# Kernel tuning notes

Hardware: AMD Instinct MI355X
Metric: run time of the kernel (lower is better)

Reference implementation:

```python
import jax, jax.numpy as jnp
import numpy as np

VOXEL_SIZE = 0.2   # matches init voxel_size
N_STEPS = 192      # fixed-step ray marching (vectorized stand-in for per-ray DDA)


def setup_inputs() -> dict:
    key = jax.random.key(0)
    k1, k2, k3, k4 = jax.random.split(key, 4)
    B, T, Z, Y, X = 1, 6, 32, 512, 512
    N = 65536
    # non-negative occupancy density (sigma)
    sigma = jax.random.uniform(k1, (B, T, Z, Y, X), jnp.float32) * 2.0
    # sensor origin near grid center per future frame, coords in (x, y, z) voxel units
    center = jnp.array([X / 2.0, Y / 2.0, Z / 2.0], jnp.float32)
    org = center + jax.random.uniform(k2, (B, T, 3), jnp.float32) * 2.0
    # point cloud endpoints uniformly inside the grid
    pcd = jax.random.uniform(k3, (B, N, 3), jnp.float32) * jnp.array([X - 1.0, Y - 1.0, Z - 1.0], jnp.float32)
    tindex = jax.random.randint(k4, (B, N), 0, T).astype(jnp.int32)
    return {"dense_occ_sigma": sigma, "future_org": org, "future_pcd": pcd, "future_tindex": tindex}


def _render(sigma, org, pcd, tindex):
    # sigma: [B,T,Z,Y,X]; org: [B,T,3]; pcd: [B,N,3]; tindex: [B,N]
    B, T, Z, Y, X = sigma.shape
    b_idx = jnp.arange(B)[:, None]                      # [B,1]
    org_pts = org[b_idx, tindex]                        # [B,N,3] origin per ray
    ray = pcd - org_pts                                 # [B,N,3]
    gt = jnp.sqrt(jnp.sum(ray * ray, axis=-1))          # [B,N] gt distance (voxel units)
    dirn = ray / jnp.maximum(gt[..., None], 1e-8)
    # midpoint samples along each ray
    frac = (jnp.arange(N_STEPS, dtype=jnp.float32) + 0.5) / N_STEPS  # [S]
    t = gt[..., None] * frac                            # [B,N,S]
    pos = org_pts[..., None, :] + dirn[..., None, :] * t[..., None]  # [B,N,S,3]
    ix = jnp.floor(pos[..., 0]).astype(jnp.int32)
    iy = jnp.floor(pos[..., 1]).astype(jnp.int32)
    iz = jnp.floor(pos[..., 2]).astype(jnp.int32)
    inside = (ix >= 0) & (ix < X) & (iy >= 0) & (iy < Y) & (iz >= 0) & (iz < Z)
    ixc = jnp.clip(ix, 0, X - 1)
    iyc = jnp.clip(iy, 0, Y - 1)
    izc = jnp.clip(iz, 0, Z - 1)
    s = sigma[b_idx[..., None], tindex[..., None], izc, iyc, ixc]    # [B,N,S] voxel gathers
    s = jnp.where(inside, s, 0.0)
    delta = (gt / N_STEPS)[..., None]                   # [B,N,1] step length
    tau = s * delta                                     # optical thickness per step
    cum = jnp.cumsum(tau, axis=-1)                      # [B,N,S]
    trans = jnp.exp(-(cum - tau))                       # transmittance before each step
    alpha = 1.0 - jnp.exp(-tau)
    w = trans * alpha                                   # termination prob per step
    # expected termination distance; residual transmittance terminates at ray end
    pred = jnp.sum(w * t, axis=-1) + jnp.exp(-cum[..., -1]) * gt
    return pred, gt


def reference(dense_occ_sigma, future_org, future_pcd, future_tindex):
    pred, gt = _render(dense_occ_sigma, future_org, future_pcd, future_tindex)
    # NaN/Inf cleanup as in the wrapper (gt masked with pred's invalid mask)
    bad = jnp.isinf(pred) | jnp.isnan(pred)
    pred = jnp.where(bad, 0.0, pred)
    gt = jnp.where(bad, 0.0, gt)
    return pred * VOXEL_SIZE, gt * VOXEL_SIZE
```

## Files before the change

### kernel.cpp

```cpp
#include <hip/hip_runtime.h>
#include <math.h>

#define TFRAMES 6
#define ZD 32
#define YD 512
#define XD 512
#define NRAYS 65536
#define NSTEPS 192
#define VOXEL 0.2f

__global__ __launch_bounds__(256) void volrender_kernel(
    const float* __restrict__ sigma,
    const float* __restrict__ org,
    const float* __restrict__ pcd,
    const int*   __restrict__ tindex,
    float*       __restrict__ out)
{
    const int lane = threadIdx.x & 63;
    const int ray  = (blockIdx.x * blockDim.x + threadIdx.x) >> 6;
    if (ray >= NRAYS) return;

    const int   t  = tindex[ray];
    const float px = pcd[ray * 3 + 0];
    const float py = pcd[ray * 3 + 1];
    const float pz = pcd[ray * 3 + 2];
    const float ox = org[t * 3 + 0];
    const float oy = org[t * 3 + 1];
    const float oz = org[t * 3 + 2];

    const float rx = px - ox, ry = py - oy, rz = pz - oz;
    float gt = sqrtf(rx * rx + ry * ry + rz * rz);
    const float invgt = 1.0f / fmaxf(gt, 1e-8f);
    const float dx = rx * invgt, dy = ry * invgt, dz = rz * invgt;
    const float delta = gt * (1.0f / NSTEPS);

    const int base = t * (ZD * YD * XD);

    float tau[3], tt[3];
#pragma unroll
    for (int j = 0; j < 3; ++j) {
        const int   s    = lane * 3 + j;
        const float frac = ((float)s + 0.5f) * (1.0f / NSTEPS);
        const float tcur = gt * frac;
        tt[j] = tcur;
        const float x = ox + dx * tcur;
        const float y = oy + dy * tcur;
        const float z = oz + dz * tcur;
        const int ix = (int)floorf(x);
        const int iy = (int)floorf(y);
        const int iz = (int)floorf(z);
        const bool inside = (ix >= 0) & (ix < XD) & (iy >= 0) & (iy < YD) &
                            (iz >= 0) & (iz < ZD);
        const int ixc = min(max(ix, 0), XD - 1);
        const int iyc = min(max(iy, 0), YD - 1);
        const int izc = min(max(iz, 0), ZD - 1);
        const float sv = sigma[base + (izc * YD + iyc) * XD + ixc];
        tau[j] = inside ? sv * delta : 0.0f;
    }

    const float p0 = tau[0];
    const float p1 = p0 + tau[1];
    const float p2 = p1 + tau[2];

    float incl = p2;
#pragma unroll
    for (int off = 1; off < 64; off <<= 1) {
        const float u = __shfl_up(incl, off);
        if (lane >= off) incl += u;
    }
    const float excl  = incl - p2;
    const float total = __shfl(incl, 63);

    const float e0 = __expf(-excl);
    const float e1 = __expf(-(excl + p0));
    const float e2 = __expf(-(excl + p1));
    const float e3 = __expf(-(excl + p2));
    float pr = (e0 - e1) * tt[0] + (e1 - e2) * tt[1] + (e2 - e3) * tt[2];

#pragma unroll
    for (int off = 32; off >= 1; off >>= 1)
        pr += __shfl_xor(pr, off);

    float pred = pr + __expf(-total) * gt;

    if (isnan(pred) || isinf(pred)) { pred = 0.0f; gt = 0.0f; }

    if (lane == 0) {
        out[ray]         = pred * VOXEL;
        out[NRAYS + ray] = gt * VOXEL;
    }
}

extern "C" void kernel_launch(void* const* d_in, const int* in_sizes, int n_in,
                              void* d_out, int out_size, void* d_ws, size_t ws_size,
                              hipStream_t stream) {
    const float* sigma  = (const float*)d_in[0];
    const float* org    = (const float*)d_in[1];
    const float* pcd    = (const float*)d_in[2];
    const int*   tindex = (const int*)d_in[3];
    float*       out    = (float*)d_out;

    const int threads = 256;
    const int blocks  = (NRAYS * 64) / threads;
    volrender_kernel<<<blocks, threads, 0, stream>>>(sigma, org, pcd, tindex, out);
}
```

Measured before the change: 329.9 us.

## Bin rays by frame and endpoint tile and remap blocks for cache locality

Adds a counting-sort pass that bins rays by time frame and coarse 64x64 XY tile of the endpoint, producing a permutation that the render kernel uses to order ray processing. Block indices are also swizzled across 8 groups so that concurrently running blocks touch spatially similar rays. The goal is better L2/MALL reuse of sigma gathers, since rays in the same frame and region sample overlapping voxels near the shared origin and endpoint. This costs four extra small kernel launches, atomics and an indirection load per ray, and only takes effect when workspace is provided.

```diff
diff --git a/kernel.cpp b/kernel.cpp
--- a/kernel.cpp
+++ b/kernel.cpp
@@ -9,16 +9,57 @@
 #define NSTEPS 192
 #define VOXEL 0.2f
 
+#define NBINS (TFRAMES * 64)
+
+
+__global__ void zero_counts_kernel(int* counts) {
+    if (threadIdx.x < NBINS) counts[threadIdx.x] = 0;
+}
+
+__device__ __forceinline__ int ray_bin(const float* pcd, const int* tindex, int i) {
+    const int   t  = tindex[i];
+    const float px = pcd[i * 3 + 0];
+    const float py = pcd[i * 3 + 1];
+    const int ex = min(7, max(0, (int)(px * (1.0f / 64.0f))));
+    const int ey = min(7, max(0, (int)(py * (1.0f / 64.0f))));
+    return (t * 8 + ey) * 8 + ex;
+}
+
+__global__ __launch_bounds__(256) void hist_kernel(
+    const float* __restrict__ pcd, const int* __restrict__ tindex, int* counts) {
+    const int i = blockIdx.x * 256 + threadIdx.x;
+    atomicAdd(&counts[ray_bin(pcd, tindex, i)], 1);
+}
+
+__global__ void prefix_kernel(const int* __restrict__ counts, int* offsets) {
+    if (threadIdx.x == 0 && blockIdx.x == 0) {
+        int acc = 0;
+        for (int b = 0; b < NBINS; ++b) { offsets[b] = acc; acc += counts[b]; }
+    }
+}
+
+__global__ __launch_bounds__(256) void scatter_kernel(
+    const float* __restrict__ pcd, const int* __restrict__ tindex,
+    int* offsets, int* __restrict__ perm) {
+    const int i = blockIdx.x * 256 + threadIdx.x;
+    const int pos = atomicAdd(&offsets[ray_bin(pcd, tindex, i)], 1);
+    perm[pos] = i;
+}
+
+
 __global__ __launch_bounds__(256) void volrender_kernel(
     const float* __restrict__ sigma,
     const float* __restrict__ org,
     const float* __restrict__ pcd,
     const int*   __restrict__ tindex,
+    const int*   __restrict__ perm,
     float*       __restrict__ out)
 {
     const int lane = threadIdx.x & 63;
-    const int ray  = (blockIdx.x * blockDim.x + threadIdx.x) >> 6;
-    if (ray >= NRAYS) return;
+    const int lb   = (blockIdx.x & 7) * 2048 + (blockIdx.x >> 3);
+    const int slot = lb * 4 + (threadIdx.x >> 6);
+    if (slot >= NRAYS) return;
+    const int ray = perm ? perm[slot] : slot;
 
     const int   t  = tindex[ray];
     const float px = pcd[ray * 3 + 0];
@@ -100,7 +141,19 @@
     const int*   tindex = (const int*)d_in[3];
     float*       out    = (float*)d_out;
 
+    const size_t need = (size_t)(NBINS * 2 + NRAYS) * sizeof(int);
+    int* perm = nullptr;
+    if (d_ws && ws_size >= need) {
+        int* counts  = (int*)d_ws;
+        int* offsets = counts + NBINS;
+        perm         = offsets + NBINS;
+        zero_counts_kernel<<<1, NBINS, 0, stream>>>(counts);
+        hist_kernel<<<NRAYS / 256, 256, 0, stream>>>(pcd, tindex, counts);
+        prefix_kernel<<<1, 64, 0, stream>>>(counts, offsets);
+        scatter_kernel<<<NRAYS / 256, 256, 0, stream>>>(pcd, tindex, offsets, perm);
+    }
+
     const int threads = 256;
     const int blocks  = (NRAYS * 64) / threads;
-    volrender_kernel<<<blocks, threads, 0, stream>>>(sigma, org, pcd, tindex, out);
+    volrender_kernel<<<blocks, threads, 0, stream>>>(sigma, org, pcd, tindex, perm, out);
 }
```

Result: slower. 371.8 us (+12.7%).
